# Kernel optimization log

Hardware: AMD Instinct MI355X
Metric: run time of the kernel (lower is better)

The kernel has to match this reference:

```python
import jax, jax.numpy as jnp
import numpy as np

NUM_HEADS = 8
ALPHA = 4.0
BN_EPS = 1e-5


def _dwconv(x, w, pad):
    # x: [B, C, H, W], w: [C, 1, kh, kw] depthwise (groups == C)
    return jax.lax.conv_general_dilated(
        x, w, window_strides=(1, 1), padding=[(pad, pad), (pad, pad)],
        dimension_numbers=('NCHW', 'OIHW', 'NCHW'),
        feature_group_count=x.shape[1])


def _forward(x, qg_w, kv_w, proj_w, proj_b, dwc_w, dwc_b, power_p, scale_p,
             enh_w, bn_gamma, bn_beta, enhance_weight, pos_enc):
    B, N, C = x.shape
    H = W = int(round(N ** 0.5))
    h = NUM_HEADS
    d = C // h

    # qg linear (no bias): [B, N, 2C] -> q, g
    qg = jnp.einsum('bnc,oc->bno', x, qg_w)
    q, g = qg[..., :C], qg[..., C:]

    # SpatialFilterEnhancer on q: depthwise 3x3 conv + BN(train) + ReLU
    qi = q.transpose(0, 2, 1).reshape(B, C, H, W)
    qe = _dwconv(qi, enh_w, pad=1)
    m = qe.mean(axis=(0, 2, 3), keepdims=True)
    var = qe.var(axis=(0, 2, 3), keepdims=True)
    qe = (qe - m) * jax.lax.rsqrt(var + BN_EPS)
    qe = qe * bn_gamma[None, :, None, None] + bn_beta[None, :, None, None]
    qe = jax.nn.relu(qe)
    q_enh = qe.reshape(B, C, N).transpose(0, 2, 1)
    q = q + enhance_weight * q_enh

    # kv linear (sr_ratio == 1 path)
    kv = jnp.einsum('bnc,oc->bno', x, kv_w)
    k, v = kv[..., :C], kv[..., C:]
    k = k + pos_enc  # learned positional encoding, shape [1, N, C]
    n = k.shape[1]

    scale = jax.nn.softplus(scale_p)              # [1, 1, C]
    power = 1.0 + ALPHA * jax.nn.sigmoid(power_p)  # [1, h, 1, d]
    q = q / scale
    k = k / scale

    # split heads: [B, h, N, d]
    q = q.reshape(B, N, h, d).transpose(0, 2, 1, 3)
    k = k.reshape(B, n, h, d).transpose(0, 2, 1, 3)
    v = v.reshape(B, n, h, d).transpose(0, 2, 1, 3)

    # power-law kernel feature maps
    q_pos = jax.nn.relu(q) ** power
    q_neg = jax.nn.relu(-q) ** power
    k_pos = jax.nn.relu(k) ** power
    k_neg = jax.nn.relu(-k) ** power
    q_sim = jnp.concatenate([q_pos, q_neg], axis=-1)   # [B, h, N, 2d]
    q_opp = jnp.concatenate([q_neg, q_pos], axis=-1)
    kf = jnp.concatenate([k_pos, k_neg], axis=-1)      # [B, h, n, 2d]
    v1, v2 = jnp.split(v, 2, axis=-1)                  # [B, h, n, d/2] each

    k_mean = kf.mean(axis=-2)  # [B, h, 2d]
    inv_n = 1.0 / n

    # sim branch
    z = 1.0 / (jnp.einsum('bhnd,bhd->bhn', q_sim, k_mean)[..., None] + 1e-6)
    kv1 = jnp.einsum('bhnd,bhne->bhde', kf, v1) * inv_n  # (n^-0.5)*(n^-0.5)
    x_sim = jnp.einsum('bhnd,bhde->bhne', q_sim, kv1) * z

    # opp branch
    z2 = 1.0 / (jnp.einsum('bhnd,bhd->bhn', q_opp, k_mean)[..., None] + 1e-6)
    kv2 = jnp.einsum('bhnd,bhne->bhde', kf, v2) * inv_n
    x_opp = jnp.einsum('bhnd,bhde->bhne', q_opp, kv2) * z2

    xa = jnp.concatenate([x_sim, x_opp], axis=-1)       # [B, h, N, d]
    xa = xa.transpose(0, 2, 1, 3).reshape(B, N, C)

    # depthwise conv positional branch on v (sr_ratio == 1 -> no interpolate)
    vimg = v.reshape(B * h, H, W, d).transpose(0, 3, 1, 2)  # [B*h, d, H, W]
    vd = _dwconv(vimg, dwc_w, pad=2) + dwc_b[None, :, None, None]
    v_out = vd.reshape(B, C, N).transpose(0, 2, 1)          # [B, N, C]

    out = (xa + v_out) * g
    out = jnp.einsum('bnc,oc->bno', out, proj_w) + proj_b
    return out


def setup_inputs() -> dict:
    key = jax.random.key(0)
    ks = jax.random.split(key, 10)
    B, N, C = 8, 3136, 512
    h = NUM_HEADS
    d = C // h
    f = lambda k, shape, s=0.02: jax.random.normal(k, shape, jnp.float32) * s
    return dict(
        x=jax.random.normal(ks[0], (B, N, C), jnp.float32),
        qg_w=f(ks[1], (2 * C, C)),
        kv_w=f(ks[2], (2 * C, C)),
        proj_w=f(ks[3], (C, C)),
        proj_b=jnp.zeros((C,), jnp.float32),
        dwc_w=f(ks[4], (d, 1, 5, 5), 0.1),
        dwc_b=jnp.zeros((d,), jnp.float32),
        power_p=f(ks[5], (1, h, 1, d), 0.1),
        scale_p=f(ks[6], (1, 1, C), 0.1),
        enh_w=f(ks[7], (C, 1, 3, 3), 0.1),
        bn_gamma=jnp.ones((C,), jnp.float32),
        bn_beta=jnp.zeros((C,), jnp.float32),
        enhance_weight=jnp.float32(0.5),
        pos_enc=f(ks[8], (1, N, C)),
    )


def reference(x, qg_w, kv_w, proj_w, proj_b, dwc_w, dwc_b, power_p, scale_p,
              enh_w, bn_gamma, bn_beta, enhance_weight, pos_enc):
    return _forward(x, qg_w, kv_w, proj_w, proj_b, dwc_w, dwc_b, power_p,
                    scale_p, enh_w, bn_gamma, bn_beta, enhance_weight, pos_enc)
```

## Files before the change

### kernel.cpp

```cpp
#include <hip/hip_runtime.h>
#include <hip/hip_bf16.h>
#include <math.h>

#define CDIM 512
#define NTOK 3136
#define BATCH 8
#define MTOT (BATCH*NTOK)
#define NHEAD 8
#define DHEAD 64
#define HW 56

typedef __attribute__((ext_vector_type(8))) short short8;
typedef __attribute__((ext_vector_type(4))) float f32x4;

__device__ __forceinline__ ushort f2bf(float f) {
    union { float f; unsigned int u; } v; v.f = f;
    unsigned int u = v.u + 0x7FFFu + ((v.u >> 16) & 1u);
    return (ushort)(u >> 16);
}
__device__ __forceinline__ float bf2f(ushort u) {
    union { unsigned int u; float f; } v; v.u = ((unsigned int)u) << 16;
    return v.f;
}

__device__ __forceinline__ void gload_lds16(const void* g, void* lds) {
    __builtin_amdgcn_global_load_lds((const __attribute__((address_space(1))) void*)g,
                                     (__attribute__((address_space(3))) void*)lds,
                                     16, 0, 0);
}

__global__ void prep_kernel(const float* __restrict__ scale_p,
                            const float* __restrict__ power_p,
                            float* __restrict__ inv_scale,
                            float* __restrict__ power) {
    int c = threadIdx.x;
    if (c < CDIM) {
        float s = log1pf(expf(scale_p[c]));
        inv_scale[c] = 1.0f / s;
        power[c] = 1.0f + 4.0f / (1.0f + expf(-power_p[c]));
    }
}

__global__ __launch_bounds__(256) void cvt_bf16_kernel(const float* __restrict__ src,
                                                       ushort* __restrict__ dst, int n4) {
    int i = blockIdx.x * 256 + threadIdx.x;
    if (i < n4) {
        float4 f = ((const float4*)src)[i];
        ushort4 o;
        o.x = f2bf(f.x); o.y = f2bf(f.y); o.z = f2bf(f.z); o.w = f2bf(f.w);
        ((ushort4*)dst)[i] = o;
    }
}

__global__ __launch_bounds__(256) void mgemm_qgkv(const ushort* __restrict__ A,
                                                  const ushort* __restrict__ Wqg,
                                                  const ushort* __restrict__ Wkv,
                                                  float* __restrict__ Qout,
                                                  float* __restrict__ Gout,
                                                  ushort* __restrict__ KFout,
                                                  ushort* __restrict__ Vout,
                                                  const float* __restrict__ pos,
                                                  const float* __restrict__ invs,
                                                  const float* __restrict__ powr) {
    __shared__ __align__(16) char smem[65536];
    ushort* At = (ushort*)smem;
    ushort* Bt = (ushort*)(smem + 32768);
    float*  Osh = (float*)smem;

    const int t = threadIdx.x;
    const int w = t >> 6, l = t & 63;
    const int wr = w >> 1, wc = w & 1;
    const int r8 = l >> 3, sl = l & 7;
    const int ss = sl ^ r8;

    const int bid = blockIdx.x;
    const int idp = (bid & 7) * 392 + (bid >> 3);
    const int mb = idp >> 4, ob = idp & 15;
    const int m0 = mb * 128;
    const ushort* Bp = (ob < 8) ? (Wqg + (size_t)ob * 128 * CDIM)
                                : (Wkv + (size_t)(ob - 8) * 128 * CDIM);

    auto stage = [&](int buf, int ks) {
        const int k0 = ks * 64;
        #pragma unroll
        for (int c = 0; c < 4; ++c) {
            int rc = (w * 4 + c) * 8 + r8;
            gload_lds16(A + (size_t)(m0 + rc) * CDIM + k0 + ss * 8, At + buf * 8192 + (w * 4 + c) * 512);
            gload_lds16(Bp + (size_t)rc * CDIM + k0 + ss * 8, Bt + buf * 8192 + (w * 4 + c) * 512);
        }
    };

    f32x4 acc[4][4] = {};
    stage(0, 0);
    __syncthreads();
    for (int ks = 0; ks < 8; ++ks) {
        int cur = ks & 1;
        if (ks < 7) stage(cur ^ 1, ks + 1);
        #pragma unroll
        for (int kk = 0; kk < 2; ++kk) {
            short8 af[4], bfr[4];
            const int sbase = kk * 4 + (l >> 4);
            #pragma unroll
            for (int i = 0; i < 4; ++i) {
                int row = wr * 64 + i * 16 + (l & 15);
                af[i] = *(const short8*)&At[cur * 8192 + row * 64 + ((sbase ^ (row & 7)) * 8)];
                int rowb = wc * 64 + i * 16 + (l & 15);
                bfr[i] = *(const short8*)&Bt[cur * 8192 + rowb * 64 + ((sbase ^ (rowb & 7)) * 8)];
            }
            #pragma unroll
            for (int i = 0; i < 4; ++i)
                #pragma unroll
                for (int j = 0; j < 4; ++j)
                    acc[i][j] = __builtin_amdgcn_mfma_f32_16x16x32_bf16(af[i], bfr[j], acc[i][j], 0, 0, 0);
        }
        __syncthreads();
    }

    #pragma unroll
    for (int i = 0; i < 4; ++i)
        #pragma unroll
        for (int j = 0; j < 4; ++j)
            #pragma unroll
            for (int rr = 0; rr < 4; ++rr)
                Osh[(wr * 64 + i * 16 + (l >> 4) * 4 + rr) * 128 + wc * 64 + j * 16 + (l & 15)] = acc[i][j][rr];
    __syncthreads();

    const int colbase = ob * 128;
    if (colbase < 512) {
        #pragma unroll
        for (int q = 0; q < 16; ++q) {
            int fi = q * 256 + t;
            int r = fi >> 5, c4 = (fi & 31) * 4;
            float4 v = *(float4*)&Osh[r * 128 + c4];
            *(float4*)&Qout[(size_t)(m0 + r) * CDIM + colbase + c4] = v;
        }
    } else if (colbase < 1024) {
        #pragma unroll
        for (int q = 0; q < 16; ++q) {
            int fi = q * 256 + t;
            int r = fi >> 5, c4 = (fi & 31) * 4;
            float4 v = *(float4*)&Osh[r * 128 + c4];
            *(float4*)&Gout[(size_t)(m0 + r) * CDIM + colbase - 512 + c4] = v;
        }
    } else if (colbase < 1536) {
        #pragma unroll
        for (int q = 0; q < 16; ++q) {
            int fi = q * 256 + t;
            int r = fi >> 5, c4 = (fi & 31) * 4;
            float4 v = *(float4*)&Osh[r * 128 + c4];
            int m = m0 + r;
            int n = m % NTOK;
            int oc = colbase - 1024 + c4;
            float4 pv = *(const float4*)&pos[(size_t)n * CDIM + oc];
            float4 iv = *(const float4*)&invs[oc];
            float4 pw = *(const float4*)&powr[oc];
            float kx0 = (v.x + pv.x) * iv.x, kx1 = (v.y + pv.y) * iv.y;
            float kx2 = (v.z + pv.z) * iv.z, kx3 = (v.w + pv.w) * iv.w;
            float t0 = __powf(fabsf(kx0), pw.x), t1 = __powf(fabsf(kx1), pw.y);
            float t2 = __powf(fabsf(kx2), pw.z), t3 = __powf(fabsf(kx3), pw.w);
            ushort4 up, un;
            up.x = kx0 > 0.f ? f2bf(t0) : 0; un.x = kx0 < 0.f ? f2bf(t0) : 0;
            up.y = kx1 > 0.f ? f2bf(t1) : 0; un.y = kx1 < 0.f ? f2bf(t1) : 0;
            up.z = kx2 > 0.f ? f2bf(t2) : 0; un.z = kx2 < 0.f ? f2bf(t2) : 0;
            up.w = kx3 > 0.f ? f2bf(t3) : 0; un.w = kx3 < 0.f ? f2bf(t3) : 0;
            ushort* dst = KFout + (size_t)m * 1024 + ((oc >> 6) << 7) + (oc & 63);
            *(ushort4*)dst = up;
            *(ushort4*)(dst + 64) = un;
        }
    } else {
        #pragma unroll
        for (int q = 0; q < 16; ++q) {
            int fi = q * 256 + t;
            int r = fi >> 5, c4 = (fi & 31) * 4;
            float4 v = *(float4*)&Osh[r * 128 + c4];
            ushort4 o;
            o.x = f2bf(v.x); o.y = f2bf(v.y); o.z = f2bf(v.z); o.w = f2bf(v.w);
            *(ushort4*)&Vout[(size_t)(m0 + r) * CDIM + colbase - 1536 + c4] = o;
        }
    }
}

__global__ __launch_bounds__(256) void mgemm_proj(const ushort* __restrict__ A,
                                                  const ushort* __restrict__ W,
                                                  float* __restrict__ out,
                                                  const float* __restrict__ pb) {
    __shared__ __align__(16) char smem[65536];
    ushort* At = (ushort*)smem;
    ushort* Bt = (ushort*)(smem + 32768);
    float*  Osh = (float*)smem;

    const int t = threadIdx.x;
    const int w = t >> 6, l = t & 63;
    const int wr = w >> 1, wc = w & 1;
    const int r8 = l >> 3, sl = l & 7;
    const int ss = sl ^ r8;

    const int bid = blockIdx.x;
    const int idp = (bid & 7) * 98 + (bid >> 3);
    const int mb = idp >> 2, ob = idp & 3;
    const int m0 = mb * 128;
    const ushort* Bp = W + (size_t)ob * 128 * CDIM;

    auto stage = [&](int buf, int ks) {
        const int k0 = ks * 64;
        #pragma unroll
        for (int c = 0; c < 4; ++c) {
            int rc = (w * 4 + c) * 8 + r8;
            gload_lds16(A + (size_t)(m0 + rc) * CDIM + k0 + ss * 8, At + buf * 8192 + (w * 4 + c) * 512);
            gload_lds16(Bp + (size_t)rc * CDIM + k0 + ss * 8, Bt + buf * 8192 + (w * 4 + c) * 512);
        }
    };

    f32x4 acc[4][4] = {};
    stage(0, 0);
    __syncthreads();
    for (int ks = 0; ks < 8; ++ks) {
        int cur = ks & 1;
        if (ks < 7) stage(cur ^ 1, ks + 1);
        #pragma unroll
        for (int kk = 0; kk < 2; ++kk) {
            short8 af[4], bfr[4];
            const int sbase = kk * 4 + (l >> 4);
            #pragma unroll
            for (int i = 0; i < 4; ++i) {
                int row = wr * 64 + i * 16 + (l & 15);
                af[i] = *(const short8*)&At[cur * 8192 + row * 64 + ((sbase ^ (row & 7)) * 8)];
                int rowb = wc * 64 + i * 16 + (l & 15);
                bfr[i] = *(const short8*)&Bt[cur * 8192 + rowb * 64 + ((sbase ^ (rowb & 7)) * 8)];
            }
            #pragma unroll
            for (int i = 0; i < 4; ++i)
                #pragma unroll
                for (int j = 0; j < 4; ++j)
                    acc[i][j] = __builtin_amdgcn_mfma_f32_16x16x32_bf16(af[i], bfr[j], acc[i][j], 0, 0, 0);
        }
        __syncthreads();
    }

    #pragma unroll
    for (int i = 0; i < 4; ++i)
        #pragma unroll
        for (int j = 0; j < 4; ++j)
            #pragma unroll
            for (int rr = 0; rr < 4; ++rr)
                Osh[(wr * 64 + i * 16 + (l >> 4) * 4 + rr) * 128 + wc * 64 + j * 16 + (l & 15)] = acc[i][j][rr];
    __syncthreads();

    const int colbase = ob * 128;
    #pragma unroll
    for (int q = 0; q < 16; ++q) {
        int fi = q * 256 + t;
        int r = fi >> 5, c4 = (fi & 31) * 4;
        float4 v = *(float4*)&Osh[r * 128 + c4];
        float4 b4 = *(const float4*)&pb[colbase + c4];
        v.x += b4.x; v.y += b4.y; v.z += b4.z; v.w += b4.w;
        *(float4*)&out[(size_t)(m0 + r) * CDIM + colbase + c4] = v;
    }
}

__global__ __launch_bounds__(256) void conv3s_kernel(const float* __restrict__ Q,
                                                     const float* __restrict__ enh_w,
                                                     float* __restrict__ QE,
                                                     float* __restrict__ ssum,
                                                     float* __restrict__ ssq) {
    const int t = threadIdx.x;
    const int c0 = t * 2;
    const int xpos = blockIdx.x;
    const int byc = blockIdx.y;
    const int b = byc >> 2, yc = byc & 3;
    const int y0 = yc * 14;

    float wgt[9][2];
    #pragma unroll
    for (int tap = 0; tap < 9; ++tap) {
        wgt[tap][0] = enh_w[c0 * 9 + tap];
        wgt[tap][1] = enh_w[(c0 + 1) * 9 + tap];
    }
    const size_t base = (size_t)b * NTOK * CDIM + c0;

    float2 win[3][3];
    auto ldrow = [&](int yy, float2* dst) {
        #pragma unroll
        for (int dx = 0; dx < 3; ++dx) {
            int xx = xpos + dx - 1;
            bool ok = (yy >= 0 && yy < HW && xx >= 0 && xx < HW);
            dst[dx] = ok ? *(const float2*)(Q + base + ((size_t)(yy * HW + xx) << 9))
                         : make_float2(0.f, 0.f);
        }
    };
    ldrow(y0 - 1, win[0]);
    ldrow(y0,     win[1]);

    float s1a = 0.f, s2a = 0.f, s1b = 0.f, s2b = 0.f;
    #pragma unroll
    for (int i = 0; i < 14; ++i) {
        int y = y0 + i;
        ldrow(y + 1, win[(i + 2) % 3]);
        float a0 = 0.f, a1 = 0.f;
        #pragma unroll
        for (int dy = 0; dy < 3; ++dy) {
            float2* row = win[(i + dy) % 3];
            #pragma unroll
            for (int dx = 0; dx < 3; ++dx) {
                a0 = fmaf(row[dx].x, wgt[dy * 3 + dx][0], a0);
                a1 = fmaf(row[dx].y, wgt[dy * 3 + dx][1], a1);
            }
        }
        *(float2*)(QE + base + ((size_t)(y * HW + xpos) << 9)) = make_float2(a0, a1);
        s1a += a0; s2a += a0 * a0;
        s1b += a1; s2b += a1 * a1;
    }
    atomicAdd(&ssum[c0], s1a);     atomicAdd(&ssq[c0], s2a);
    atomicAdd(&ssum[c0 + 1], s1b); atomicAdd(&ssq[c0 + 1], s2b);
}

__global__ void bnprep_kernel(const float* __restrict__ ssum, const float* __restrict__ ssq,
                              const float* __restrict__ bn_g, const float* __restrict__ bn_b,
                              float* __restrict__ achan, float* __restrict__ bchan) {
    int c = threadIdx.x;
    if (c < CDIM) {
        const float invM = 1.0f / (float)MTOT;
        float mean = ssum[c] * invM;
        float var  = ssq[c] * invM - mean * mean;
        float a = bn_g[c] * rsqrtf(var + 1e-5f);
        achan[c] = a;
        bchan[c] = bn_b[c] - mean * a;
    }
}

__global__ __launch_bounds__(256) void kvred4_kernel(const ushort* __restrict__ KF,
                                                     const ushort* __restrict__ Vbf,
                                                     float* __restrict__ PKV) {
    const int bh = blockIdx.x, chunk = blockIdx.y;
    const int b = bh >> 3, head = bh & 7;
    const int t = threadIdx.x;
    const int w = t >> 6, l = t & 63;
    const int lr = l & 15;
    const int ns = (l >> 4) * 8;

    const int nbase = b * NTOK + chunk * 448;
    const ushort* kf0 = KF  + ((size_t)(nbase + ns)) * 1024 + head * 128 + (w * 32 + lr);
    const ushort* vb0 = Vbf + ((size_t)(nbase + ns)) * 512  + head * 64  + lr;

    short8 ones;
    #pragma unroll
    for (int j = 0; j < 8; ++j) ones[j] = (lr == 0) ? (short)0x3F80 : (short)0;

    f32x4 acc[2][5] = {};
    for (int tile = 0; tile < 14; ++tile) {
        union { uint u[4]; short8 s; } ua[2], ub[4];
        #pragma unroll
        for (int i = 0; i < 2; ++i) {
            #pragma unroll
            for (int j = 0; j < 4; ++j) {
                uint lo = kf0[i * 16 + (size_t)(2 * j) * 1024];
                uint hi = kf0[i * 16 + (size_t)(2 * j + 1) * 1024];
                ua[i].u[j] = lo | (hi << 16);
            }
        }
        #pragma unroll
        for (int j5 = 0; j5 < 4; ++j5) {
            #pragma unroll
            for (int j = 0; j < 4; ++j) {
                uint lo = vb0[j5 * 16 + (size_t)(2 * j) * 512];
                uint hi = vb0[j5 * 16 + (size_t)(2 * j + 1) * 512];
                ub[j5].u[j] = lo | (hi << 16);
            }
        }
        #pragma unroll
        for (int i = 0; i < 2; ++i) {
            #pragma unroll
            for (int j5 = 0; j5 < 4; ++j5)
                acc[i][j5] = __builtin_amdgcn_mfma_f32_16x16x32_bf16(ua[i].s, ub[j5].s, acc[i][j5], 0, 0, 0);
            acc[i][4] = __builtin_amdgcn_mfma_f32_16x16x32_bf16(ua[i].s, ones, acc[i][4], 0, 0, 0);
        }
        kf0 += (size_t)32 * 1024;
        vb0 += (size_t)32 * 512;
    }
    size_t base = ((size_t)(chunk * 64 + bh)) * 8320;
    #pragma unroll
    for (int i = 0; i < 2; ++i) {
        int d0 = w * 32 + i * 16 + (l >> 4) * 4;
        #pragma unroll
        for (int j = 0; j < 5; ++j) {
            int e = j * 16 + lr;
            if (j < 4 || e == 64)
                *(f32x4*)(PKV + base + (size_t)e * 128 + d0) = acc[i][j];
        }
    }
}

__global__ __launch_bounds__(256) void kvreduce2_kernel(const float* __restrict__ PKV,
                                                        ushort* __restrict__ kvTbf) {
    int gid = blockIdx.x * 256 + threadIdx.x;
    const float inv_n = 1.0f / (float)NTOK;
    int bh = gid / 10240;
    int r  = gid - bh * 10240;
    int row = r >> 7, dcol = r & 127;
    int dlog = (((dcol >> 3) ^ (row & 7)) << 3) | (dcol & 7);
    float s = 0.f;
    if (row < 64) {
        int dsel = (row >= 32) ? (dlog ^ 64) : dlog;
        #pragma unroll
        for (int c = 0; c < 7; ++c) s += PKV[(size_t)c * 532480 + (size_t)bh * 8320 + row * 128 + dsel];
    } else if (row < 66) {
        int dsel = (row == 65) ? (dlog ^ 64) : dlog;
        #pragma unroll
        for (int c = 0; c < 7; ++c) s += PKV[(size_t)c * 532480 + (size_t)bh * 8320 + 64 * 128 + dsel];
    }
    kvTbf[gid] = (row < 66) ? f2bf(s * inv_n) : (ushort)0;
}

__global__ __launch_bounds__(256) void attn_mfma_kernel(const float* __restrict__ Q,
                                                        const float* __restrict__ QE,
                                                        const ushort* __restrict__ kvTbf,
                                                        const float* __restrict__ power,
                                                        const float* __restrict__ achan,
                                                        const float* __restrict__ bchan,
                                                        const float* __restrict__ invs,
                                                        const float* __restrict__ ewp,
                                                        ushort* __restrict__ ATTbf) {
    __shared__ ushort QF[64 * 128];
    __shared__ ushort BT[80 * 128];
    const int bh = blockIdx.x, tb = blockIdx.y;
    const int b = bh >> 3, head = bh & 7;
    const int t = threadIdx.x;
    const int w = t >> 6, l = t & 63;

    #pragma unroll
    for (int i = 0; i < 5; ++i) {
        int f = i * 256 + t;
        gload_lds16(kvTbf + (size_t)bh * 10240 + f * 8, BT + f * 8);
    }

    const int c = l, hc = head * 64 + c;
    const float p = power[hc];
    const float ac = achan[hc], bc = bchan[hc], iv = invs[hc], ew = ewp[0];
    #pragma unroll
    for (int i = 0; i < 16; ++i) {
        int tok = i * 4 + w;
        size_t off = ((size_t)(b * NTOK + tb * 64 + tok)) * CDIM + hc;
        float q = Q[off];
        float qe = QE[off];
        q = (q + ew * fmaxf(fmaf(ac, qe, bc), 0.f)) * iv;
        float ax = fabsf(q);
        float tp = ax > 0.f ? __powf(ax, p) : 0.f;
        float qp = q > 0.f ? tp : 0.f;
        float qn = q < 0.f ? tp : 0.f;
        int sw = tok & 7;
        QF[tok * 128 + (((c >> 3) ^ sw) * 8) + (c & 7)]       = f2bf(qp);
        QF[tok * 128 + ((((c >> 3) + 8) ^ sw) * 8) + (c & 7)] = f2bf(qn);
    }
    __syncthreads();

    f32x4 acc[5] = {};
    #pragma unroll
    for (int kk = 0; kk < 4; ++kk) {
        int sbase = kk * 4 + (l >> 4);
        int rowa = w * 16 + (l & 15);
        short8 af = *(const short8*)&QF[rowa * 128 + ((sbase ^ (rowa & 7)) * 8)];
        #pragma unroll
        for (int j = 0; j < 5; ++j) {
            int rowb = j * 16 + (l & 15);
            short8 bf = *(const short8*)&BT[rowb * 128 + ((sbase ^ (rowb & 7)) * 8)];
            acc[j] = __builtin_amdgcn_mfma_f32_16x16x32_bf16(af, bf, acc[j], 0, 0, 0);
        }
    }
    __syncthreads();

    ushort* Oout = QF;
    #pragma unroll
    for (int rr = 0; rr < 4; ++rr) {
        float ssim = __shfl(acc[4][rr], (l & 48));
        float sopp = __shfl(acc[4][rr], (l & 48) + 1);
        float zs = 1.f / (ssim + 1e-6f);
        float zo = 1.f / (sopp + 1e-6f);
        int tokl = w * 16 + (l >> 4) * 4 + rr;
        #pragma unroll
        for (int j = 0; j < 4; ++j) {
            int e = j * 16 + (l & 15);
            Oout[tokl * 64 + e] = f2bf(acc[j][rr] * (j < 2 ? zs : zo));
        }
    }
    __syncthreads();

    #pragma unroll
    for (int i = 0; i < 2; ++i) {
        int idx = i * 256 + t;
        int tokl = idx >> 3, ch = (idx & 7) * 8;
        short8 vv = *(short8*)&Oout[tokl * 64 + ch];
        *(short8*)&ATTbf[((size_t)(b * NTOK + tb * 64 + tokl)) * CDIM + head * 64 + ch] = vv;
    }
}

__global__ __launch_bounds__(256) void voutg2_kernel(const ushort* __restrict__ Vbf,
                                                     const ushort* __restrict__ ATTbf,
                                                     const float* __restrict__ G,
                                                     const float* __restrict__ dwc_w,
                                                     const float* __restrict__ dwc_b,
                                                     ushort* __restrict__ PRE) {
    const int t = threadIdx.x;
    const int c0 = t * 2;
    const int xpos = blockIdx.x;
    const int byc = blockIdx.y;
    const int b = byc >> 2, yc = byc & 3;
    const int y0 = yc * 14;
    const int dch = c0 & 63;

    float wgt[25][2];
    #pragma unroll
    for (int tap = 0; tap < 25; ++tap) {
        wgt[tap][0] = dwc_w[dch * 25 + tap];
        wgt[tap][1] = dwc_w[(dch + 1) * 25 + tap];
    }
    const float bias0 = dwc_b[dch], bias1 = dwc_b[dch + 1];
    const size_t base = (size_t)b * NTOK * CDIM + c0;

    float2 win[5][5];
    auto ldrow = [&](int yy, float2* dst) {
        #pragma unroll
        for (int dx = 0; dx < 5; ++dx) {
            int xx = xpos + dx - 2;
            bool ok = (yy >= 0 && yy < HW && xx >= 0 && xx < HW);
            if (ok) {
                ushort2 uv = *(const ushort2*)(Vbf + base + ((size_t)(yy * HW + xx) << 9));
                dst[dx] = make_float2(bf2f(uv.x), bf2f(uv.y));
            } else {
                dst[dx] = make_float2(0.f, 0.f);
            }
        }
    };
    ldrow(y0 - 2, win[0]);
    ldrow(y0 - 1, win[1]);
    ldrow(y0,     win[2]);
    ldrow(y0 + 1, win[3]);

    #pragma unroll
    for (int i = 0; i < 14; ++i) {
        int y = y0 + i;
        ldrow(y + 2, win[(i + 4) % 5]);
        float a0 = bias0, a1 = bias1;
        #pragma unroll
        for (int dy = 0; dy < 5; ++dy) {
            float2* row = win[(i + dy) % 5];
            #pragma unroll
            for (int dx = 0; dx < 5; ++dx) {
                a0 = fmaf(row[dx].x, wgt[dy * 5 + dx][0], a0);
                a1 = fmaf(row[dx].y, wgt[dy * 5 + dx][1], a1);
            }
        }
        size_t oidx = base + ((size_t)(y * HW + xpos) << 9);
        ushort2 au = *(const ushort2*)(ATTbf + oidx);
        float2 g   = *(const float2*)(G + oidx);
        ushort2 o;
        o.x = f2bf((bf2f(au.x) + a0) * g.x);
        o.y = f2bf((bf2f(au.y) + a1) * g.y);
        *(ushort2*)(PRE + oidx) = o;
    }
}

extern "C" void kernel_launch(void* const* d_in, const int* in_sizes, int n_in,
                              void* d_out, int out_size, void* d_ws, size_t ws_size,
                              hipStream_t stream) {
    const float* x      = (const float*)d_in[0];
    const float* qg_w   = (const float*)d_in[1];
    const float* kv_w   = (const float*)d_in[2];
    const float* proj_w = (const float*)d_in[3];
    const float* proj_b = (const float*)d_in[4];
    const float* dwc_w  = (const float*)d_in[5];
    const float* dwc_b  = (const float*)d_in[6];
    const float* power_p= (const float*)d_in[7];
    const float* scale_p= (const float*)d_in[8];
    const float* enh_w  = (const float*)d_in[9];
    const float* bn_g   = (const float*)d_in[10];
    const float* bn_b   = (const float*)d_in[11];
    const float* ew_p   = (const float*)d_in[12];
    const float* pos    = (const float*)d_in[13];

    const size_t NELEM = (size_t)MTOT * CDIM;
    float* ws    = (float*)d_ws;
    float* Qb    = ws;
    float* Gb    = ws + NELEM;
    float* Kb    = ws + 2 * NELEM;
    float* Vb    = ws + 3 * NELEM;
    float* QEb   = ws + 4 * NELEM;
    float* SMALL = ws + 5 * NELEM;
    float* ssum  = SMALL;
    float* ssq   = SMALL + 512;
    ushort* kvTbf= (ushort*)(SMALL + 9216);
    float* invs  = SMALL + 533504;
    float* powr  = SMALL + 534016;
    float* achan = SMALL + 534528;
    float* bchan = SMALL + 535040;
    ushort* Wqg  = (ushort*)(SMALL + 535552);
    ushort* Wkv  = (ushort*)(SMALL + 797696);
    ushort* Wproj= (ushort*)(SMALL + 1059840);

    ushort* Xbf  = (ushort*)QEb;
    ushort* KFbf = (ushort*)Kb;
    ushort* Vbf  = (ushort*)Vb;
    float* PKV   = Kb + NELEM / 2;
    ushort* ATTbf= (ushort*)(Vb + NELEM / 2);
    ushort* PREbf= (ushort*)Kb;

    hipMemsetAsync(SMALL, 0, (size_t)1024 * sizeof(float), stream);

    prep_kernel<<<1, 512, 0, stream>>>(scale_p, power_p, invs, powr);

    cvt_bf16_kernel<<<12544, 256, 0, stream>>>(x, Xbf, 3211264);
    cvt_bf16_kernel<<<512, 256, 0, stream>>>(qg_w, Wqg, 131072);
    cvt_bf16_kernel<<<512, 256, 0, stream>>>(kv_w, Wkv, 131072);
    cvt_bf16_kernel<<<256, 256, 0, stream>>>(proj_w, Wproj, 65536);

    mgemm_qgkv<<<3136, 256, 0, stream>>>(Xbf, Wqg, Wkv, Qb, Gb, KFbf, Vbf, pos, invs, powr);

    dim3 cgrid(56, 32);
    conv3s_kernel<<<cgrid, 256, 0, stream>>>(Qb, enh_w, QEb, ssum, ssq);
    bnprep_kernel<<<1, 512, 0, stream>>>(ssum, ssq, bn_g, bn_b, achan, bchan);

    kvred4_kernel<<<dim3(64, 7), 256, 0, stream>>>(KFbf, Vbf, PKV);
    kvreduce2_kernel<<<2560, 256, 0, stream>>>(PKV, kvTbf);

    attn_mfma_kernel<<<dim3(64, 49), 256, 0, stream>>>(Qb, QEb, kvTbf, powr,
                                                       achan, bchan, invs, ew_p, ATTbf);

    voutg2_kernel<<<cgrid, 256, 0, stream>>>(Vbf, ATTbf, Gb, dwc_w, dwc_b, PREbf);

    mgemm_proj<<<784, 256, 0, stream>>>(PREbf, Wproj, (float*)d_out, proj_b);
}
```

Before: 498.5 us.

## Store Q, G, QE intermediates in bf16 and halve GEMM LDS tiles

The Q, G and enhanced-Q intermediates are now stored as bf16 instead of fp32, and the conv, attention and output-gate kernels read and write bf16. This roughly halves the memory traffic for those tensors, which dominate the pipeline's global memory use. Both GEMMs switch to a 32-wide K step with 32 KB of LDS, a new swizzle, and an epilogue written in two halves through a padded staging buffer. The smaller LDS footprint should raise occupancy, at the cost of twice as many K iterations and barriers, plus extra rounding error in Q, G and QE.

```diff
diff --git a/kernel.cpp b/kernel.cpp
--- a/kernel.cpp
+++ b/kernel.cpp
@@ -55,23 +55,21 @@
 __global__ __launch_bounds__(256) void mgemm_qgkv(const ushort* __restrict__ A,
                                                   const ushort* __restrict__ Wqg,
                                                   const ushort* __restrict__ Wkv,
-                                                  float* __restrict__ Qout,
-                                                  float* __restrict__ Gout,
+                                                  ushort* __restrict__ Qout,
+                                                  ushort* __restrict__ Gout,
                                                   ushort* __restrict__ KFout,
                                                   ushort* __restrict__ Vout,
                                                   const float* __restrict__ pos,
                                                   const float* __restrict__ invs,
                                                   const float* __restrict__ powr) {
-    __shared__ __align__(16) char smem[65536];
+    __shared__ __align__(16) char smem[32768];
     ushort* At = (ushort*)smem;
-    ushort* Bt = (ushort*)(smem + 32768);
+    ushort* Bt = (ushort*)(smem + 16384);
     float*  Osh = (float*)smem;
 
     const int t = threadIdx.x;
     const int w = t >> 6, l = t & 63;
     const int wr = w >> 1, wc = w & 1;
-    const int r8 = l >> 3, sl = l & 7;
-    const int ss = sl ^ r8;
 
     const int bid = blockIdx.x;
     const int idp = (bid & 7) * 392 + (bid >> 3);
@@ -81,102 +79,99 @@
                                 : (Wkv + (size_t)(ob - 8) * 128 * CDIM);
 
     auto stage = [&](int buf, int ks) {
-        const int k0 = ks * 64;
-        #pragma unroll
-        for (int c = 0; c < 4; ++c) {
-            int rc = (w * 4 + c) * 8 + r8;
-            gload_lds16(A + (size_t)(m0 + rc) * CDIM + k0 + ss * 8, At + buf * 8192 + (w * 4 + c) * 512);
-            gload_lds16(Bp + (size_t)rc * CDIM + k0 + ss * 8, Bt + buf * 8192 + (w * 4 + c) * 512);
+        const int k0 = ks * 32;
+        #pragma unroll
+        for (int i = 0; i < 2; ++i) {
+            int f = t + i * 256;
+            int r = f >> 2, ps = f & 3;
+            int ls = ps ^ ((r >> 2) & 3);
+            gload_lds16(A + (size_t)(m0 + r) * CDIM + k0 + ls * 8, At + buf * 4096 + f * 8);
+            gload_lds16(Bp + (size_t)r * CDIM + k0 + ls * 8, Bt + buf * 4096 + f * 8);
         }
     };
 
     f32x4 acc[4][4] = {};
+    const int psl = (l >> 4) ^ ((l >> 2) & 3);
     stage(0, 0);
     __syncthreads();
-    for (int ks = 0; ks < 8; ++ks) {
+    for (int ks = 0; ks < 16; ++ks) {
         int cur = ks & 1;
-        if (ks < 7) stage(cur ^ 1, ks + 1);
-        #pragma unroll
-        for (int kk = 0; kk < 2; ++kk) {
-            short8 af[4], bfr[4];
-            const int sbase = kk * 4 + (l >> 4);
-            #pragma unroll
-            for (int i = 0; i < 4; ++i) {
-                int row = wr * 64 + i * 16 + (l & 15);
-                af[i] = *(const short8*)&At[cur * 8192 + row * 64 + ((sbase ^ (row & 7)) * 8)];
-                int rowb = wc * 64 + i * 16 + (l & 15);
-                bfr[i] = *(const short8*)&Bt[cur * 8192 + rowb * 64 + ((sbase ^ (rowb & 7)) * 8)];
-            }
+        if (ks < 15) stage(cur ^ 1, ks + 1);
+        short8 af[4], bfr[4];
+        #pragma unroll
+        for (int i = 0; i < 4; ++i) {
+            int row = wr * 64 + i * 16 + (l & 15);
+            af[i] = *(const short8*)&At[cur * 4096 + row * 32 + psl * 8];
+            int rowb = wc * 64 + i * 16 + (l & 15);
+            bfr[i] = *(const short8*)&Bt[cur * 4096 + rowb * 32 + psl * 8];
+        }
+        #pragma unroll
+        for (int i = 0; i < 4; ++i)
+            #pragma unroll
+            for (int j = 0; j < 4; ++j)
+                acc[i][j] = __builtin_amdgcn_mfma_f32_16x16x32_bf16(af[i], bfr[j], acc[i][j], 0, 0, 0);
+        __syncthreads();
+    }
+
+    const int colbase = ob * 128;
+    #pragma unroll
+    for (int p = 0; p < 2; ++p) {
+        if (wr == p) {
             #pragma unroll
             for (int i = 0; i < 4; ++i)
                 #pragma unroll
                 for (int j = 0; j < 4; ++j)
-                    acc[i][j] = __builtin_amdgcn_mfma_f32_16x16x32_bf16(af[i], bfr[j], acc[i][j], 0, 0, 0);
+                    #pragma unroll
+                    for (int rr = 0; rr < 4; ++rr) {
+                        int r = i * 16 + (l >> 4) * 4 + rr;
+                        int c = wc * 64 + j * 16 + (l & 15);
+                        int pc = (c + ((r & 4) << 2)) & 127;
+                        Osh[r * 128 + pc] = acc[i][j][rr];
+                    }
         }
         __syncthreads();
-    }
-
-    #pragma unroll
-    for (int i = 0; i < 4; ++i)
-        #pragma unroll
-        for (int j = 0; j < 4; ++j)
-            #pragma unroll
-            for (int rr = 0; rr < 4; ++rr)
-                Osh[(wr * 64 + i * 16 + (l >> 4) * 4 + rr) * 128 + wc * 64 + j * 16 + (l & 15)] = acc[i][j][rr];
-    __syncthreads();
-
-    const int colbase = ob * 128;
-    if (colbase < 512) {
-        #pragma unroll
-        for (int q = 0; q < 16; ++q) {
+        #pragma unroll
+        for (int q = 0; q < 8; ++q) {
             int fi = q * 256 + t;
-            int r = fi >> 5, c4 = (fi & 31) * 4;
-            float4 v = *(float4*)&Osh[r * 128 + c4];
-            *(float4*)&Qout[(size_t)(m0 + r) * CDIM + colbase + c4] = v;
-        }
-    } else if (colbase < 1024) {
-        #pragma unroll
-        for (int q = 0; q < 16; ++q) {
-            int fi = q * 256 + t;
-            int r = fi >> 5, c4 = (fi & 31) * 4;
-            float4 v = *(float4*)&Osh[r * 128 + c4];
-            *(float4*)&Gout[(size_t)(m0 + r) * CDIM + colbase - 512 + c4] = v;
-        }
-    } else if (colbase < 1536) {
-        #pragma unroll
-        for (int q = 0; q < 16; ++q) {
-            int fi = q * 256 + t;
-            int r = fi >> 5, c4 = (fi & 31) * 4;
-            float4 v = *(float4*)&Osh[r * 128 + c4];
+            int rl = fi >> 5;
+            int r = p * 64 + rl;
+            int c4 = (fi & 31) * 4;
+            int pc = (c4 + ((rl & 4) << 2)) & 127;
+            float4 v = *(float4*)&Osh[rl * 128 + pc];
             int m = m0 + r;
-            int n = m % NTOK;
-            int oc = colbase - 1024 + c4;
-            float4 pv = *(const float4*)&pos[(size_t)n * CDIM + oc];
-            float4 iv = *(const float4*)&invs[oc];
-            float4 pw = *(const float4*)&powr[oc];
-            float kx0 = (v.x + pv.x) * iv.x, kx1 = (v.y + pv.y) * iv.y;
-            float kx2 = (v.z + pv.z) * iv.z, kx3 = (v.w + pv.w) * iv.w;
-            float t0 = __powf(fabsf(kx0), pw.x), t1 = __powf(fabsf(kx1), pw.y);
-            float t2 = __powf(fabsf(kx2), pw.z), t3 = __powf(fabsf(kx3), pw.w);
-            ushort4 up, un;
-            up.x = kx0 > 0.f ? f2bf(t0) : 0; un.x = kx0 < 0.f ? f2bf(t0) : 0;
-            up.y = kx1 > 0.f ? f2bf(t1) : 0; un.y = kx1 < 0.f ? f2bf(t1) : 0;
-            up.z = kx2 > 0.f ? f2bf(t2) : 0; un.z = kx2 < 0.f ? f2bf(t2) : 0;
-            up.w = kx3 > 0.f ? f2bf(t3) : 0; un.w = kx3 < 0.f ? f2bf(t3) : 0;
-            ushort* dst = KFout + (size_t)m * 1024 + ((oc >> 6) << 7) + (oc & 63);
-            *(ushort4*)dst = up;
-            *(ushort4*)(dst + 64) = un;
-        }
-    } else {
-        #pragma unroll
-        for (int q = 0; q < 16; ++q) {
-            int fi = q * 256 + t;
-            int r = fi >> 5, c4 = (fi & 31) * 4;
-            float4 v = *(float4*)&Osh[r * 128 + c4];
-            ushort4 o;
-            o.x = f2bf(v.x); o.y = f2bf(v.y); o.z = f2bf(v.z); o.w = f2bf(v.w);
-            *(ushort4*)&Vout[(size_t)(m0 + r) * CDIM + colbase - 1536 + c4] = o;
-        }
+            if (colbase < 512) {
+                ushort4 o;
+                o.x = f2bf(v.x); o.y = f2bf(v.y); o.z = f2bf(v.z); o.w = f2bf(v.w);
+                *(ushort4*)&Qout[(size_t)m * CDIM + colbase + c4] = o;
+            } else if (colbase < 1024) {
+                ushort4 o;
+                o.x = f2bf(v.x); o.y = f2bf(v.y); o.z = f2bf(v.z); o.w = f2bf(v.w);
+                *(ushort4*)&Gout[(size_t)m * CDIM + colbase - 512 + c4] = o;
+            } else if (colbase < 1536) {
+                int n = m % NTOK;
+                int oc = colbase - 1024 + c4;
+                float4 pv = *(const float4*)&pos[(size_t)n * CDIM + oc];
+                float4 iv = *(const float4*)&invs[oc];
+                float4 pw = *(const float4*)&powr[oc];
+                float kx0 = (v.x + pv.x) * iv.x, kx1 = (v.y + pv.y) * iv.y;
+                float kx2 = (v.z + pv.z) * iv.z, kx3 = (v.w + pv.w) * iv.w;
+                float t0 = __powf(fabsf(kx0), pw.x), t1 = __powf(fabsf(kx1), pw.y);
+                float t2 = __powf(fabsf(kx2), pw.z), t3 = __powf(fabsf(kx3), pw.w);
+                ushort4 up, un;
+                up.x = kx0 > 0.f ? f2bf(t0) : 0; un.x = kx0 < 0.f ? f2bf(t0) : 0;
+                up.y = kx1 > 0.f ? f2bf(t1) : 0; un.y = kx1 < 0.f ? f2bf(t1) : 0;
+                up.z = kx2 > 0.f ? f2bf(t2) : 0; un.z = kx2 < 0.f ? f2bf(t2) : 0;
+                up.w = kx3 > 0.f ? f2bf(t3) : 0; un.w = kx3 < 0.f ? f2bf(t3) : 0;
+                ushort* dst = KFout + (size_t)m * 1024 + ((oc >> 6) << 7) + (oc & 63);
+                *(ushort4*)dst = up;
+                *(ushort4*)(dst + 64) = un;
+            } else {
+                ushort4 o;
+                o.x = f2bf(v.x); o.y = f2bf(v.y); o.z = f2bf(v.z); o.w = f2bf(v.w);
+                *(ushort4*)&Vout[(size_t)m * CDIM + colbase - 1536 + c4] = o;
+            }
+        }
+        __syncthreads();
     }
 }
 
@@ -184,16 +179,14 @@
                                                   const ushort* __restrict__ W,
                                                   float* __restrict__ out,
                                                   const float* __restrict__ pb) {
-    __shared__ __align__(16) char smem[65536];
+    __shared__ __align__(16) char smem[32768];
     ushort* At = (ushort*)smem;
-    ushort* Bt = (ushort*)(smem + 32768);
+    ushort* Bt = (ushort*)(smem + 16384);
     float*  Osh = (float*)smem;
 
     const int t = threadIdx.x;
     const int w = t >> 6, l = t & 63;
     const int wr = w >> 1, wc = w & 1;
-    const int r8 = l >> 3, sl = l & 7;
-    const int ss = sl ^ r8;
 
     const int bid = blockIdx.x;
     const int idp = (bid & 7) * 98 + (bid >> 3);
@@ -202,65 +195,76 @@
     const ushort* Bp = W + (size_t)ob * 128 * CDIM;
 
     auto stage = [&](int buf, int ks) {
-        const int k0 = ks * 64;
-        #pragma unroll
-        for (int c = 0; c < 4; ++c) {
-            int rc = (w * 4 + c) * 8 + r8;
-            gload_lds16(A + (size_t)(m0 + rc) * CDIM + k0 + ss * 8, At + buf * 8192 + (w * 4 + c) * 512);
-            gload_lds16(Bp + (size_t)rc * CDIM + k0 + ss * 8, Bt + buf * 8192 + (w * 4 + c) * 512);
+        const int k0 = ks * 32;
+        #pragma unroll
+        for (int i = 0; i < 2; ++i) {
+            int f = t + i * 256;
+            int r = f >> 2, ps = f & 3;
+            int ls = ps ^ ((r >> 2) & 3);
+            gload_lds16(A + (size_t)(m0 + r) * CDIM + k0 + ls * 8, At + buf * 4096 + f * 8);
+            gload_lds16(Bp + (size_t)r * CDIM + k0 + ls * 8, Bt + buf * 4096 + f * 8);
         }
     };
 
     f32x4 acc[4][4] = {};
+    const int psl = (l >> 4) ^ ((l >> 2) & 3);
     stage(0, 0);
     __syncthreads();
-    for (int ks = 0; ks < 8; ++ks) {
+    for (int ks = 0; ks < 16; ++ks) {
         int cur = ks & 1;
-        if (ks < 7) stage(cur ^ 1, ks + 1);
-        #pragma unroll
-        for (int kk = 0; kk < 2; ++kk) {
-            short8 af[4], bfr[4];
-            const int sbase = kk * 4 + (l >> 4);
-            #pragma unroll
-            for (int i = 0; i < 4; ++i) {
-                int row = wr * 64 + i * 16 + (l & 15);
-                af[i] = *(const short8*)&At[cur * 8192 + row * 64 + ((sbase ^ (row & 7)) * 8)];
-                int rowb = wc * 64 + i * 16 + (l & 15);
-                bfr[i] = *(const short8*)&Bt[cur * 8192 + rowb * 64 + ((sbase ^ (rowb & 7)) * 8)];
-            }
+        if (ks < 15) stage(cur ^ 1, ks + 1);
+        short8 af[4], bfr[4];
+        #pragma unroll
+        for (int i = 0; i < 4; ++i) {
+            int row = wr * 64 + i * 16 + (l & 15);
+            af[i] = *(const short8*)&At[cur * 4096 + row * 32 + psl * 8];
+            int rowb = wc * 64 + i * 16 + (l & 15);
+            bfr[i] = *(const short8*)&Bt[cur * 4096 + rowb * 32 + psl * 8];
+        }
+        #pragma unroll
+        for (int i = 0; i < 4; ++i)
+            #pragma unroll
+            for (int j = 0; j < 4; ++j)
+                acc[i][j] = __builtin_amdgcn_mfma_f32_16x16x32_bf16(af[i], bfr[j], acc[i][j], 0, 0, 0);
+        __syncthreads();
+    }
+
+    const int colbase = ob * 128;
+    #pragma unroll
+    for (int p = 0; p < 2; ++p) {
+        if (wr == p) {
             #pragma unroll
             for (int i = 0; i < 4; ++i)
                 #pragma unroll
                 for (int j = 0; j < 4; ++j)
-                    acc[i][j] = __builtin_amdgcn_mfma_f32_16x16x32_bf16(af[i], bfr[j], acc[i][j], 0, 0, 0);
+                    #pragma unroll
+                    for (int rr = 0; rr < 4; ++rr) {
+                        int r = i * 16 + (l >> 4) * 4 + rr;
+                        int c = wc * 64 + j * 16 + (l & 15);
+                        int pc = (c + ((r & 4) << 2)) & 127;
+                        Osh[r * 128 + pc] = acc[i][j][rr];
+                    }
         }
         __syncthreads();
-    }
-
-    #pragma unroll
-    for (int i = 0; i < 4; ++i)
-        #pragma unroll
-        for (int j = 0; j < 4; ++j)
-            #pragma unroll
-            for (int rr = 0; rr < 4; ++rr)
-                Osh[(wr * 64 + i * 16 + (l >> 4) * 4 + rr) * 128 + wc * 64 + j * 16 + (l & 15)] = acc[i][j][rr];
-    __syncthreads();
-
-    const int colbase = ob * 128;
-    #pragma unroll
-    for (int q = 0; q < 16; ++q) {
-        int fi = q * 256 + t;
-        int r = fi >> 5, c4 = (fi & 31) * 4;
-        float4 v = *(float4*)&Osh[r * 128 + c4];
-        float4 b4 = *(const float4*)&pb[colbase + c4];
-        v.x += b4.x; v.y += b4.y; v.z += b4.z; v.w += b4.w;
-        *(float4*)&out[(size_t)(m0 + r) * CDIM + colbase + c4] = v;
-    }
-}
-
-__global__ __launch_bounds__(256) void conv3s_kernel(const float* __restrict__ Q,
+        #pragma unroll
+        for (int q = 0; q < 8; ++q) {
+            int fi = q * 256 + t;
+            int rl = fi >> 5;
+            int r = p * 64 + rl;
+            int c4 = (fi & 31) * 4;
+            int pc = (c4 + ((rl & 4) << 2)) & 127;
+            float4 v = *(float4*)&Osh[rl * 128 + pc];
+            float4 b4 = *(const float4*)&pb[colbase + c4];
+            v.x += b4.x; v.y += b4.y; v.z += b4.z; v.w += b4.w;
+            *(float4*)&out[(size_t)(m0 + r) * CDIM + colbase + c4] = v;
+        }
+        __syncthreads();
+    }
+}
+
+__global__ __launch_bounds__(256) void conv3s_kernel(const ushort* __restrict__ Qbf,
                                                      const float* __restrict__ enh_w,
-                                                     float* __restrict__ QE,
+                                                     ushort* __restrict__ QEbf,
                                                      float* __restrict__ ssum,
                                                      float* __restrict__ ssq) {
     const int t = threadIdx.x;
@@ -284,8 +288,12 @@
         for (int dx = 0; dx < 3; ++dx) {
             int xx = xpos + dx - 1;
             bool ok = (yy >= 0 && yy < HW && xx >= 0 && xx < HW);
-            dst[dx] = ok ? *(const float2*)(Q + base + ((size_t)(yy * HW + xx) << 9))
-                         : make_float2(0.f, 0.f);
+            if (ok) {
+                ushort2 uv = *(const ushort2*)(Qbf + base + ((size_t)(yy * HW + xx) << 9));
+                dst[dx] = make_float2(bf2f(uv.x), bf2f(uv.y));
+            } else {
+                dst[dx] = make_float2(0.f, 0.f);
+            }
         }
     };
     ldrow(y0 - 1, win[0]);
@@ -306,7 +314,8 @@
                 a1 = fmaf(row[dx].y, wgt[dy * 3 + dx][1], a1);
             }
         }
-        *(float2*)(QE + base + ((size_t)(y * HW + xpos) << 9)) = make_float2(a0, a1);
+        ushort2 o; o.x = f2bf(a0); o.y = f2bf(a1);
+        *(ushort2*)(QEbf + base + ((size_t)(y * HW + xpos) << 9)) = o;
         s1a += a0; s2a += a0 * a0;
         s1b += a1; s2b += a1 * a1;
     }
@@ -411,8 +420,8 @@
     kvTbf[gid] = (row < 66) ? f2bf(s * inv_n) : (ushort)0;
 }
 
-__global__ __launch_bounds__(256) void attn_mfma_kernel(const float* __restrict__ Q,
-                                                        const float* __restrict__ QE,
+__global__ __launch_bounds__(256) void attn_mfma_kernel(const ushort* __restrict__ Qbf,
+                                                        const ushort* __restrict__ QEbf,
                                                         const ushort* __restrict__ kvTbf,
                                                         const float* __restrict__ power,
                                                         const float* __restrict__ achan,
@@ -440,8 +449,8 @@
     for (int i = 0; i < 16; ++i) {
         int tok = i * 4 + w;
         size_t off = ((size_t)(b * NTOK + tb * 64 + tok)) * CDIM + hc;
-        float q = Q[off];
-        float qe = QE[off];
+        float q = bf2f(Qbf[off]);
+        float qe = bf2f(QEbf[off]);
         q = (q + ew * fmaxf(fmaf(ac, qe, bc), 0.f)) * iv;
         float ax = fabsf(q);
         float tp = ax > 0.f ? __powf(ax, p) : 0.f;
@@ -495,7 +504,7 @@
 
 __global__ __launch_bounds__(256) void voutg2_kernel(const ushort* __restrict__ Vbf,
                                                      const ushort* __restrict__ ATTbf,
-                                                     const float* __restrict__ G,
+                                                     const ushort* __restrict__ Gbf,
                                                      const float* __restrict__ dwc_w,
                                                      const float* __restrict__ dwc_b,
                                                      ushort* __restrict__ PRE) {
@@ -551,10 +560,10 @@
         }
         size_t oidx = base + ((size_t)(y * HW + xpos) << 9);
         ushort2 au = *(const ushort2*)(ATTbf + oidx);
-        float2 g   = *(const float2*)(G + oidx);
+        ushort2 gu = *(const ushort2*)(Gbf + oidx);
         ushort2 o;
-        o.x = f2bf((bf2f(au.x) + a0) * g.x);
-        o.y = f2bf((bf2f(au.y) + a1) * g.y);
+        o.x = f2bf((bf2f(au.x) + a0) * bf2f(gu.x));
+        o.y = f2bf((bf2f(au.y) + a1) * bf2f(gu.y));
         *(ushort2*)(PRE + oidx) = o;
     }
 }
@@ -579,11 +588,15 @@
 
     const size_t NELEM = (size_t)MTOT * CDIM;
     float* ws    = (float*)d_ws;
-    float* Qb    = ws;
-    float* Gb    = ws + NELEM;
-    float* Kb    = ws + 2 * NELEM;
-    float* Vb    = ws + 3 * NELEM;
-    float* QEb   = ws + 4 * NELEM;
+    ushort* Qbf  = (ushort*)ws;
+    ushort* Gbf  = (ushort*)(ws + NELEM);
+    float*  PKV  = ws + NELEM + NELEM / 2;
+    ushort* KFbf = (ushort*)(ws + 2 * NELEM);
+    ushort* PREbf= (ushort*)(ws + 2 * NELEM);
+    ushort* Vbf  = (ushort*)(ws + 3 * NELEM);
+    ushort* ATTbf= (ushort*)(ws + 3 * NELEM + NELEM / 2);
+    ushort* Xbf  = (ushort*)(ws + 4 * NELEM);
+    ushort* QEbf = (ushort*)(ws + 4 * NELEM);
     float* SMALL = ws + 5 * NELEM;
     float* ssum  = SMALL;
     float* ssq   = SMALL + 512;
@@ -596,13 +609,6 @@
     ushort* Wkv  = (ushort*)(SMALL + 797696);
     ushort* Wproj= (ushort*)(SMALL + 1059840);
 
-    ushort* Xbf  = (ushort*)QEb;
-    ushort* KFbf = (ushort*)Kb;
-    ushort* Vbf  = (ushort*)Vb;
-    float* PKV   = Kb + NELEM / 2;
-    ushort* ATTbf= (ushort*)(Vb + NELEM / 2);
-    ushort* PREbf= (ushort*)Kb;
-
     hipMemsetAsync(SMALL, 0, (size_t)1024 * sizeof(float), stream);
 
     prep_kernel<<<1, 512, 0, stream>>>(scale_p, power_p, invs, powr);
@@ -612,19 +618,19 @@
     cvt_bf16_kernel<<<512, 256, 0, stream>>>(kv_w, Wkv, 131072);
     cvt_bf16_kernel<<<256, 256, 0, stream>>>(proj_w, Wproj, 65536);
 
-    mgemm_qgkv<<<3136, 256, 0, stream>>>(Xbf, Wqg, Wkv, Qb, Gb, KFbf, Vbf, pos, invs, powr);
+    mgemm_qgkv<<<3136, 256, 0, stream>>>(Xbf, Wqg, Wkv, Qbf, Gbf, KFbf, Vbf, pos, invs, powr);
 
     dim3 cgrid(56, 32);
-    conv3s_kernel<<<cgrid, 256, 0, stream>>>(Qb, enh_w, QEb, ssum, ssq);
+    conv3s_kernel<<<cgrid, 256, 0, stream>>>(Qbf, enh_w, QEbf, ssum, ssq);
     bnprep_kernel<<<1, 512, 0, stream>>>(ssum, ssq, bn_g, bn_b, achan, bchan);
 
     kvred4_kernel<<<dim3(64, 7), 256, 0, stream>>>(KFbf, Vbf, PKV);
     kvreduce2_kernel<<<2560, 256, 0, stream>>>(PKV, kvTbf);
 
-    attn_mfma_kernel<<<dim3(64, 49), 256, 0, stream>>>(Qb, QEb, kvTbf, powr,
+    attn_mfma_kernel<<<dim3(64, 49), 256, 0, stream>>>(Qbf, QEbf, kvTbf, powr,
                                                        achan, bchan, invs, ew_p, ATTbf);
 
-    voutg2_kernel<<<cgrid, 256, 0, stream>>>(Vbf, ATTbf, Gb, dwc_w, dwc_b, PREbf);
+    voutg2_kernel<<<cgrid, 256, 0, stream>>>(Vbf, ATTbf, Gbf, dwc_w, dwc_b, PREbf);
 
     mgemm_proj<<<784, 256, 0, stream>>>(PREbf, Wproj, (float*)d_out, proj_b);
 }
```

New measurement: 506.5 us. No clear change (+1.6%).
